# Kernel tuning notes

Measured on AMD Instinct MI355X. Metric: run time of the kernel, lower is better.

The kernel has to match this reference:

```python
import jax, jax.numpy as jnp
import numpy as np

ITER = 18  # prop_time


def _conv3x3(x, w, b):
    # NCHW conv, stride 1, pad 1 (conv_offset_aff)
    y = jax.lax.conv_general_dilated(x, w, window_strides=(1, 1),
                                     padding=((1, 1), (1, 1)),
                                     dimension_numbers=('NCHW', 'OIHW', 'NCHW'))
    return y + b[None, :, None, None]


def _bilinear(img, py, px):
    # img: [H,W]; py/px: [9,H,W] fractional sample coords; zero outside bounds
    H, W = img.shape
    y0 = jnp.floor(py)
    x0 = jnp.floor(px)
    ty = py - y0
    tx = px - x0

    def gather(yf, xf):
        valid = (yf >= 0) & (yf <= H - 1) & (xf >= 0) & (xf <= W - 1)
        yc = jnp.clip(yf, 0, H - 1).astype(jnp.int32)
        xc = jnp.clip(xf, 0, W - 1).astype(jnp.int32)
        return jnp.where(valid, img[yc, xc], 0.0)

    v00 = gather(y0, x0)
    v01 = gather(y0, x0 + 1)
    v10 = gather(y0 + 1, x0)
    v11 = gather(y0 + 1, x0 + 1)
    return (1 - ty) * ((1 - tx) * v00 + tx * v01) + ty * ((1 - tx) * v10 + tx * v11)


def _deform_conv(feat, offset, mask, w9, bias):
    # modulated deformable 3x3 conv, 1 channel, stride 1, pad 1, dil 1
    # offset: [B,18,H,W] in (dy,dx) pairs per kernel tap (torchvision layout)
    B, _, H, W = feat.shape
    off = offset.reshape(B, 9, 2, H, W)
    ky = (jnp.arange(9) // 3 - 1).astype(feat.dtype)  # kernel row offsets
    kx = (jnp.arange(9) % 3 - 1).astype(feat.dtype)   # kernel col offsets
    ys = jnp.arange(H, dtype=feat.dtype)[:, None]
    xs = jnp.arange(W, dtype=feat.dtype)[None, :]
    py = ys[None, None] + ky[None, :, None, None] + off[:, :, 0]  # [B,9,H,W]
    px = xs[None, None] + kx[None, :, None, None] + off[:, :, 1]
    sampled = jax.vmap(_bilinear)(feat[:, 0], py, px)  # [B,9,H,W]
    out = jnp.einsum('bkhw,bkhw,k->bhw', sampled, mask, w9) + bias[0]
    return out[:, None]  # [B,1,H,W]


def _forward(feat_init, guidance, confidence, feat_fix, conv_w, conv_b, w, b):
    conf = jnp.sign(feat_fix) * jax.nn.sigmoid(confidence)
    oa = _conv3x3(guidance, conv_w, conv_b)            # [B,27,H,W]
    offset1 = oa[:, :18].astype(jnp.float16)           # .half() in torch
    aff1 = jax.nn.softmax(oa[:, 18:], axis=1).astype(jnp.float16)
    off_f = offset1.astype(jnp.float32)                # .float() in loop
    aff_f = aff1.astype(jnp.float32)
    w9 = w.reshape(9)

    def step(fr, _):
        fr = (1 - conf) * _deform_conv(fr, off_f, aff_f, w9, b) + conf * feat_fix
        return fr, fr

    pred, list_feat = jax.lax.scan(step, feat_init.astype(jnp.float32), None, length=ITER)
    return pred, list_feat, offset1, aff1


def setup_inputs() -> dict:
    key = jax.random.key(0)
    ks = jax.random.split(key, 6)
    B, H, W = 2, 352, 1216
    feat_init = jax.random.normal(ks[0], (B, 1, H, W), jnp.float32)
    guidance = jax.random.normal(ks[1], (B, 9, H, W), jnp.float32)
    confidence = jax.random.normal(ks[2], (B, 1, H, W), jnp.float32)
    feat_fix = jax.random.normal(ks[3], (B, 1, H, W), jnp.float32)
    # conv_offset_aff params (zero-init in source; small random for a non-trivial baseline)
    conv_w = jax.random.normal(ks[4], (27, 9, 3, 3), jnp.float32) * 0.05
    conv_b = jax.random.normal(ks[5], (27,), jnp.float32) * 0.01
    w = jnp.ones((1, 1, 3, 3), jnp.float32)   # fixed deform-conv weight
    b = jnp.zeros((1,), jnp.float32)          # fixed deform-conv bias
    return {'feat_init': feat_init, 'guidance': guidance, 'confidence': confidence,
            'feat_fix': feat_fix, 'conv_w': conv_w, 'conv_b': conv_b, 'w': w, 'b': b}


def reference(feat_init, guidance, confidence, feat_fix, conv_w, conv_b, w, b):
    return _forward(feat_init, guidance, confidence, feat_fix, conv_w, conv_b, w, b)
```

## Files before the change

kernel.cpp:

```cpp
#include <hip/hip_runtime.h>
#include <hip/hip_fp16.h>

#define HH 352
#define WW 1216
#define HW (HH*WW)
#define NPIX (2*HW)
#define NITER 18
#define PACK_BYTES ((size_t)NPIX * 64)

#define SEGW 256
#define NSEGC ((WW + SEGW - 1) / SEGW)
#define AROW_B 208
#define A_BYTES (256 * AROW_B)
#define B_OFF A_BYTES
#define LDS_BYTES (A_BYTES + 32 * AROW_B)
#define OAROW_B 152

#define SEG 256
#define XHALO 6
#define YHALO 4
#define PROWS 4
#define TROWS (PROWS + 9)
#define TCOLS (SEG + 2*XHALO)
#define NSEG ((WW + SEG - 1) / SEG)

typedef __attribute__((ext_vector_type(8))) short short8;
typedef __attribute__((ext_vector_type(4))) float f32x4;

__device__ __forceinline__ unsigned short f2bf(float f) {
    unsigned u = __float_as_uint(f);
    unsigned r = (u + 0x7fffu + ((u >> 16) & 1u)) >> 16;
    return (unsigned short)r;
}

__global__ __launch_bounds__(256) void conv_mfma_kernel(
    const float* __restrict__ g,
    const float* __restrict__ cw,
    const float* __restrict__ cb,
    const float* __restrict__ confidence,
    const float* __restrict__ feat_fix,
    float* __restrict__ out_off,
    float* __restrict__ out_aff,
    uint4* __restrict__ packed)
{
    __shared__ char lds[LDS_BYTES];

    const int tid = threadIdx.x;
    const int bid = blockIdx.x;
    const int seg = bid % NSEGC;
    const int y   = (bid / NSEGC) % HH;
    const int b   = bid / (NSEGC * HH);
    const int xs  = seg * SEGW;
    const int x   = xs + tid;

    for (int i = tid; i < 32 * 48; i += 256) {
        int n = i / 48;
        int kp = i - n * 48;
        unsigned v = 0;
        if (n < 27) {
            const float* wrow = cw + n * 81;
            int k0 = kp * 2;
            unsigned short h0 = (k0 < 81) ? f2bf(wrow[k0]) : (unsigned short)0;
            unsigned short h1 = (k0 + 1 < 81) ? f2bf(wrow[k0 + 1]) : (unsigned short)0;
            v = (unsigned)h0 | ((unsigned)h1 << 16);
        }
        *(unsigned*)(lds + B_OFF + n * AROW_B + kp * 4) = v;
    }

    {
        const float* gb = g + (size_t)b * 9 * HW;
        unsigned au[48];
#pragma unroll
        for (int j = 0; j < 48; ++j) au[j] = 0;
#pragma unroll
        for (int ci = 0; ci < 9; ++ci)
#pragma unroll
            for (int ty = 0; ty < 3; ++ty) {
                const int row = y + ty - 1;
                const bool vr = ((unsigned)row < HH);
                const float* rp = gb + (size_t)ci * HW + (size_t)(vr ? row : 0) * WW;
                const int cx = xs + tid - 1;
                float L = (vr && (unsigned)cx < WW) ? rp[cx] : 0.f;
                float M = (vr && (unsigned)(cx + 1) < WW) ? rp[cx + 1] : 0.f;
                float R = (vr && (unsigned)(cx + 2) < WW) ? rp[cx + 2] : 0.f;
                const int k = ci * 9 + ty * 3;
                au[(k) >> 1]     |= ((unsigned)f2bf(L)) << (((k) & 1) * 16);
                au[(k + 1) >> 1] |= ((unsigned)f2bf(M)) << (((k + 1) & 1) * 16);
                au[(k + 2) >> 1] |= ((unsigned)f2bf(R)) << (((k + 2) & 1) * 16);
            }
        char* arow = lds + tid * AROW_B;
#pragma unroll
        for (int j = 0; j < 12; ++j)
            *(uint4*)(arow + 16 * j) =
                make_uint4(au[4 * j], au[4 * j + 1], au[4 * j + 2], au[4 * j + 3]);
    }
    __syncthreads();

    const int w = tid >> 6, l = tid & 63;
    const int lrow = l & 15;
    const int lk = (l >> 4) * 8;
    f32x4 acc[4][2];
#pragma unroll
    for (int mt = 0; mt < 4; ++mt)
#pragma unroll
        for (int nt = 0; nt < 2; ++nt)
            acc[mt][nt] = (f32x4){0.f, 0.f, 0.f, 0.f};

#pragma unroll
    for (int kk = 0; kk < 3; ++kk) {
        const int ko = kk * 32 + lk;
        short8 bb0 = *(const short8*)(lds + B_OFF + lrow * AROW_B + ko * 2);
        short8 bb1 = *(const short8*)(lds + B_OFF + (lrow + 16) * AROW_B + ko * 2);
#pragma unroll
        for (int mt = 0; mt < 4; ++mt) {
            short8 aa = *(const short8*)(lds + (w * 64 + mt * 16 + lrow) * AROW_B + ko * 2);
            acc[mt][0] = __builtin_amdgcn_mfma_f32_16x16x32_bf16(aa, bb0, acc[mt][0], 0, 0, 0);
            acc[mt][1] = __builtin_amdgcn_mfma_f32_16x16x32_bf16(aa, bb1, acc[mt][1], 0, 0, 0);
        }
    }
    __syncthreads();

#pragma unroll
    for (int mt = 0; mt < 4; ++mt)
#pragma unroll
        for (int nt = 0; nt < 2; ++nt)
#pragma unroll
            for (int reg = 0; reg < 4; ++reg) {
                int px = w * 64 + mt * 16 + (l >> 4) * 4 + reg;
                int ch = nt * 16 + lrow;
                *(float*)(lds + px * OAROW_B + ch * 4) = acc[mt][nt][reg];
            }
    __syncthreads();

    if (x >= WW) return;
    const int r = y * WW + x;
    const int p = b * HW + r;

    float oa[27];
    {
        const char* orow = lds + tid * OAROW_B;
#pragma unroll
        for (int j = 0; j < 13; ++j) {
            float2 v = *(const float2*)(orow + 8 * j);
            oa[2 * j] = v.x;
            if (2 * j + 1 < 27) oa[2 * j + 1] = v.y;
        }
        oa[26] = *(const float*)(orow + 26 * 4);
#pragma unroll
        for (int c = 0; c < 27; ++c) oa[c] += cb[c];
    }

    __half h[28];
#pragma unroll
    for (int c = 0; c < 18; ++c) h[c] = __float2half(oa[c]);

    float m = oa[18];
#pragma unroll
    for (int c = 19; c < 27; ++c) m = fmaxf(m, oa[c]);
    float e[9], s = 0.f;
#pragma unroll
    for (int k = 0; k < 9; ++k) { e[k] = expf(oa[18 + k] - m); s += e[k]; }
    float inv = 1.f / s;
#pragma unroll
    for (int k = 0; k < 9; ++k) h[18 + k] = __float2half(e[k] * inv);
    h[27] = __float2half(0.f);

#pragma unroll
    for (int c = 0; c < 18; ++c)
        out_off[(size_t)b * 18 * HW + (size_t)c * HW + r] = __half2float(h[c]);
#pragma unroll
    for (int k = 0; k < 9; ++k)
        out_aff[(size_t)b * 9 * HW + (size_t)k * HW + r] = __half2float(h[18 + k]);

    if (packed) {
        float cf = confidence[p];
        float ff = feat_fix[p];
        float sg = (ff > 0.f) ? 1.f : ((ff < 0.f) ? -1.f : 0.f);
        float conf = sg / (1.f + expf(-cf));

        unsigned uu[16];
#pragma unroll
        for (int i = 0; i < 14; ++i)
            uu[i] = (unsigned)__half_as_ushort(h[2 * i]) |
                    ((unsigned)__half_as_ushort(h[2 * i + 1]) << 16);
        uu[14] = __float_as_uint(1.f - conf);
        uu[15] = __float_as_uint(conf * ff);

        uint4* dst = packed + (size_t)p * 4;
        dst[0] = make_uint4(uu[0], uu[1], uu[2], uu[3]);
        dst[1] = make_uint4(uu[4], uu[5], uu[6], uu[7]);
        dst[2] = make_uint4(uu[8], uu[9], uu[10], uu[11]);
        dst[3] = make_uint4(uu[12], uu[13], uu[14], uu[15]);
    }
}

__global__ __launch_bounds__(256) void prop4_kernel(
    const float* __restrict__ src,
    float* __restrict__ dst,
    const uint4* __restrict__ packed,
    const float* __restrict__ w9,
    const float* __restrict__ biasp,
    float* __restrict__ out_pred)
{
    __shared__ float tile[TROWS * TCOLS];

    const int xs = blockIdx.x * SEG;
    const int y0 = blockIdx.y * PROWS;
    const int b  = blockIdx.z;
    const float* sf = src + (size_t)b * HW;

    for (int i = threadIdx.x; i < TROWS * TCOLS; i += 256) {
        int rr = i / TCOLS;
        int cc = i - rr * TCOLS;
        int gy = y0 - YHALO + rr;
        int gx = xs - XHALO + cc;
        float v = 0.f;
        if ((unsigned)gy < HH && (unsigned)gx < WW)
            v = sf[(size_t)gy * WW + gx];
        tile[i] = v;
    }
    __syncthreads();

    const int x = xs + threadIdx.x;
    if (x >= WW) return;
    const float bias = biasp[0];

#pragma unroll 1
    for (int ty = 0; ty < PROWS; ++ty) {
        const int y = y0 + ty;
        const int r = y * WW + x;
        const int p = b * HW + r;

        const uint4* pk = packed + (size_t)p * 4;
        uint4 q0 = pk[0], q1 = pk[1], q2 = pk[2], q3 = pk[3];
        unsigned uu[14] = {q0.x, q0.y, q0.z, q0.w, q1.x, q1.y, q1.z, q1.w,
                           q2.x, q2.y, q2.z, q2.w, q3.x, q3.y};
        float hv[27];
#pragma unroll
        for (int i = 0; i < 13; ++i) {
            hv[2 * i]     = __half2float(__ushort_as_half((unsigned short)(uu[i] & 0xffff)));
            hv[2 * i + 1] = __half2float(__ushort_as_half((unsigned short)(uu[i] >> 16)));
        }
        hv[26] = __half2float(__ushort_as_half((unsigned short)(uu[13] & 0xffff)));
        float cm1 = __uint_as_float(q3.z);
        float cff = __uint_as_float(q3.w);

        float acc = 0.f;
#pragma unroll
        for (int k = 0; k < 9; ++k) {
            float py = (float)y + (float)(k / 3 - 1) + hv[2 * k];
            float px = (float)x + (float)(k % 3 - 1) + hv[2 * k + 1];
            float y0f = floorf(py), x0f = floorf(px);
            float tyf = py - y0f, txf = px - x0f;
            int iy = (int)y0f, ix = (int)x0f;

            int ly = iy - y0 + YHALO;
            int lx = ix - xs + XHALO;
            float v00, v01, v10, v11;
            if ((unsigned)ly < (TROWS - 1) && (unsigned)lx < (TCOLS - 1)) {
                const float* t0 = &tile[ly * TCOLS + lx];
                v00 = t0[0];     v01 = t0[1];
                v10 = t0[TCOLS]; v11 = t0[TCOLS + 1];
            } else {
                bool vy0 = ((unsigned)iy < HH), vy1 = ((unsigned)(iy + 1) < HH);
                bool vx0 = ((unsigned)ix < WW), vx1 = ((unsigned)(ix + 1) < WW);
                v00 = (vy0 && vx0) ? sf[(size_t)iy * WW + ix] : 0.f;
                v01 = (vy0 && vx1) ? sf[(size_t)iy * WW + ix + 1] : 0.f;
                v10 = (vy1 && vx0) ? sf[(size_t)(iy + 1) * WW + ix] : 0.f;
                v11 = (vy1 && vx1) ? sf[(size_t)(iy + 1) * WW + ix + 1] : 0.f;
            }
            float top = (1.f - txf) * v00 + txf * v01;
            float bot = (1.f - txf) * v10 + txf * v11;
            float sv = (1.f - tyf) * top + tyf * bot;
            acc = fmaf(sv * hv[18 + k], w9[k], acc);
        }
        float dc = acc + bias;
        float fr = fmaf(cm1, dc, cff);

        dst[p] = fr;
        if (out_pred) out_pred[p] = fr;
    }
}

__global__ __launch_bounds__(256) void prop_kernel(
    const float* __restrict__ src,
    float* __restrict__ dst,
    const float* __restrict__ off,
    const float* __restrict__ aff,
    const float* __restrict__ confidence,
    const float* __restrict__ feat_fix,
    const float* __restrict__ w9,
    const float* __restrict__ biasp,
    float* __restrict__ out_pred)
{
    int p = blockIdx.x * 256 + threadIdx.x;
    if (p >= NPIX) return;
    int b = p / HW;
    int r = p - b * HW;
    int y = r / WW;
    int x = r - y * WW;

    const float* offb = off + (size_t)b * 18 * HW + r;
    const float* affb = aff + (size_t)b * 9 * HW + r;
    const float* sf = src + (size_t)b * HW;

    float acc = 0.f;
#pragma unroll
    for (int k = 0; k < 9; ++k) {
        float dy = offb[(size_t)(2 * k) * HW];
        float dx = offb[(size_t)(2 * k + 1) * HW];
        float af = affb[(size_t)k * HW];
        float py = (float)y + (float)(k / 3 - 1) + dy;
        float px = (float)x + (float)(k % 3 - 1) + dx;
        float y0f = floorf(py), x0f = floorf(px);
        float ty = py - y0f, tx = px - x0f;
        int iy = (int)y0f, ix = (int)x0f;
        bool vy0 = ((unsigned)iy < HH), vy1 = ((unsigned)(iy + 1) < HH);
        bool vx0 = ((unsigned)ix < WW), vx1 = ((unsigned)(ix + 1) < WW);
        float v00 = (vy0 && vx0) ? sf[(size_t)iy * WW + ix] : 0.f;
        float v01 = (vy0 && vx1) ? sf[(size_t)iy * WW + ix + 1] : 0.f;
        float v10 = (vy1 && vx0) ? sf[(size_t)(iy + 1) * WW + ix] : 0.f;
        float v11 = (vy1 && vx1) ? sf[(size_t)(iy + 1) * WW + ix + 1] : 0.f;
        float top = (1.f - tx) * v00 + tx * v01;
        float bot = (1.f - tx) * v10 + tx * v11;
        float sv = (1.f - ty) * top + ty * bot;
        acc = fmaf(sv * af, w9[k], acc);
    }
    float dc = acc + biasp[0];

    float cf = confidence[p];
    float ffv = feat_fix[p];
    float sg = (ffv > 0.f) ? 1.f : ((ffv < 0.f) ? -1.f : 0.f);
    float conf = sg / (1.f + expf(-cf));
    float fr = (1.f - conf) * dc + conf * ffv;

    dst[p] = fr;
    if (out_pred) out_pred[p] = fr;
}

extern "C" void kernel_launch(void* const* d_in, const int* in_sizes, int n_in,
                              void* d_out, int out_size, void* d_ws, size_t ws_size,
                              hipStream_t stream) {
    const float* feat_init  = (const float*)d_in[0];
    const float* guidance   = (const float*)d_in[1];
    const float* confidence = (const float*)d_in[2];
    const float* feat_fix   = (const float*)d_in[3];
    const float* conv_w     = (const float*)d_in[4];
    const float* conv_b     = (const float*)d_in[5];
    const float* w          = (const float*)d_in[6];
    const float* bias       = (const float*)d_in[7];

    float* outf = (float*)d_out;
    float* out_pred = outf;
    float* out_list = outf + (size_t)NPIX;
    float* out_off  = outf + (size_t)19 * NPIX;
    float* out_aff  = outf + (size_t)37 * NPIX;

    bool use_pack = (ws_size >= PACK_BYTES);
    uint4* packed = use_pack ? (uint4*)d_ws : nullptr;

    conv_mfma_kernel<<<NSEGC * HH * 2, 256, 0, stream>>>(
        guidance, conv_w, conv_b, confidence, feat_fix,
        out_off, out_aff, packed);

    dim3 pgrid(NSEG, HH / PROWS, 2);
    int blocks = (NPIX + 255) / 256;
    const float* src = feat_init;
    for (int it = 0; it < NITER; ++it) {
        float* dstf = out_list + (size_t)it * NPIX;
        float* predp = (it == NITER - 1) ? out_pred : nullptr;
        if (use_pack) {
            prop4_kernel<<<pgrid, 256, 0, stream>>>(
                src, dstf, packed, w, bias, predp);
        } else {
            prop_kernel<<<blocks, 256, 0, stream>>>(
                src, dstf, out_off, out_aff, confidence, feat_fix, w, bias, predp);
        }
        src = dstf;
    }
}
```

Before: 372.8 us.

## Fold weights and bias into packed data, double prop rows, use packed bf16 converts

The conv kernel now uses the hardware v_cvt_pk_bf16_f32 instruction and a fast interior path without bounds checks. It also pre-multiplies the affinity by the deform weights and folds the bias into the packed constant, which removes per-iteration weight loads and multiplies from the propagation kernel. The propagation kernel processes 8 rows per block instead of 4, which reduces halo overhead. It also loads tiles row-wise, reads LDS pairs as float2 and uses an FMA-form lerp. Rounding changes slightly because the weight product is stored in fp16 and the bilinear blend uses FMAs.

```diff
diff --git a/kernel.cpp b/kernel.cpp
--- a/kernel.cpp
+++ b/kernel.cpp
@@ -19,7 +19,7 @@
 #define SEG 256
 #define XHALO 6
 #define YHALO 4
-#define PROWS 4
+#define PROWS 8
 #define TROWS (PROWS + 9)
 #define TCOLS (SEG + 2*XHALO)
 #define NSEG ((WW + SEG - 1) / SEG)
@@ -27,10 +27,16 @@
 typedef __attribute__((ext_vector_type(8))) short short8;
 typedef __attribute__((ext_vector_type(4))) float f32x4;
 
-__device__ __forceinline__ unsigned short f2bf(float f) {
-    unsigned u = __float_as_uint(f);
-    unsigned r = (u + 0x7fffu + ((u >> 16) & 1u)) >> 16;
-    return (unsigned short)r;
+__device__ __forceinline__ unsigned cvt_pk_bf16(float lo, float hi) {
+    unsigned r;
+    asm("v_cvt_pk_bf16_f32 %0, %1, %2" : "=v"(r) : "v"(lo), "v"(hi));
+    return r;
+}
+
+__device__ __forceinline__ float2 lds2(const float* p) {
+    float2 v;
+    __builtin_memcpy(&v, p, 8);
+    return v;
 }
 
 __global__ __launch_bounds__(256) void conv_mfma_kernel(
@@ -39,6 +45,8 @@
     const float* __restrict__ cb,
     const float* __restrict__ confidence,
     const float* __restrict__ feat_fix,
+    const float* __restrict__ w9,
+    const float* __restrict__ biasp,
     float* __restrict__ out_off,
     float* __restrict__ out_aff,
     uint4* __restrict__ packed)
@@ -60,9 +68,9 @@
         if (n < 27) {
             const float* wrow = cw + n * 81;
             int k0 = kp * 2;
-            unsigned short h0 = (k0 < 81) ? f2bf(wrow[k0]) : (unsigned short)0;
-            unsigned short h1 = (k0 + 1 < 81) ? f2bf(wrow[k0 + 1]) : (unsigned short)0;
-            v = (unsigned)h0 | ((unsigned)h1 << 16);
+            float f0 = (k0 < 81) ? wrow[k0] : 0.f;
+            float f1 = (k0 + 1 < 81) ? wrow[k0 + 1] : 0.f;
+            v = cvt_pk_bf16(f0, f1);
         }
         *(unsigned*)(lds + B_OFF + n * AROW_B + kp * 4) = v;
     }
@@ -72,22 +80,53 @@
         unsigned au[48];
 #pragma unroll
         for (int j = 0; j < 48; ++j) au[j] = 0;
-#pragma unroll
-        for (int ci = 0; ci < 9; ++ci)
-#pragma unroll
-            for (int ty = 0; ty < 3; ++ty) {
-                const int row = y + ty - 1;
-                const bool vr = ((unsigned)row < HH);
-                const float* rp = gb + (size_t)ci * HW + (size_t)(vr ? row : 0) * WW;
-                const int cx = xs + tid - 1;
-                float L = (vr && (unsigned)cx < WW) ? rp[cx] : 0.f;
-                float M = (vr && (unsigned)(cx + 1) < WW) ? rp[cx + 1] : 0.f;
-                float R = (vr && (unsigned)(cx + 2) < WW) ? rp[cx + 2] : 0.f;
-                const int k = ci * 9 + ty * 3;
-                au[(k) >> 1]     |= ((unsigned)f2bf(L)) << (((k) & 1) * 16);
-                au[(k + 1) >> 1] |= ((unsigned)f2bf(M)) << (((k + 1) & 1) * 16);
-                au[(k + 2) >> 1] |= ((unsigned)f2bf(R)) << (((k + 2) & 1) * 16);
+        float held = 0.f;
+
+        bool interior = (y >= 1) & (y <= HH - 2) & (x >= 1) & (x <= WW - 2);
+        if (interior) {
+            const float* c0 = gb + (size_t)(y - 1) * WW + (x - 1);
+#pragma unroll
+            for (int ci = 0; ci < 9; ++ci) {
+                const float* cp = c0 + (size_t)ci * HW;
+#pragma unroll
+                for (int ty = 0; ty < 3; ++ty) {
+                    float L = cp[ty * WW], M = cp[ty * WW + 1], R = cp[ty * WW + 2];
+                    const int k = ci * 9 + ty * 3;
+                    if ((k & 1) == 0) {
+                        au[k >> 1] = cvt_pk_bf16(L, M);
+                        held = R;
+                    } else {
+                        au[(k - 1) >> 1] = cvt_pk_bf16(held, L);
+                        au[(k + 1) >> 1] = cvt_pk_bf16(M, R);
+                    }
+                }
             }
+        } else {
+#pragma unroll
+            for (int ci = 0; ci < 9; ++ci) {
+                const float* cp = gb + (size_t)ci * HW;
+#pragma unroll
+                for (int ty = 0; ty < 3; ++ty) {
+                    const int row = y + ty - 1;
+                    const bool vr = ((unsigned)row < HH);
+                    const float* rp = cp + (size_t)(vr ? row : 0) * WW;
+                    const int cx = x - 1;
+                    float L = (vr && (unsigned)cx < WW) ? rp[cx] : 0.f;
+                    float M = (vr && (unsigned)(cx + 1) < WW) ? rp[cx + 1] : 0.f;
+                    float R = (vr && (unsigned)(cx + 2) < WW) ? rp[cx + 2] : 0.f;
+                    const int k = ci * 9 + ty * 3;
+                    if ((k & 1) == 0) {
+                        au[k >> 1] = cvt_pk_bf16(L, M);
+                        held = R;
+                    } else {
+                        au[(k - 1) >> 1] = cvt_pk_bf16(held, L);
+                        au[(k + 1) >> 1] = cvt_pk_bf16(M, R);
+                    }
+                }
+            }
+        }
+        au[40] = cvt_pk_bf16(held, 0.f);
+
         char* arow = lds + tid * AROW_B;
 #pragma unroll
         for (int j = 0; j < 12; ++j)
@@ -150,7 +189,7 @@
         for (int c = 0; c < 27; ++c) oa[c] += cb[c];
     }
 
-    __half h[28];
+    __half h[27];
 #pragma unroll
     for (int c = 0; c < 18; ++c) h[c] = __float2half(oa[c]);
 
@@ -163,7 +202,6 @@
     float inv = 1.f / s;
 #pragma unroll
     for (int k = 0; k < 9; ++k) h[18 + k] = __float2half(e[k] * inv);
-    h[27] = __float2half(0.f);
 
 #pragma unroll
     for (int c = 0; c < 18; ++c)
@@ -177,14 +215,26 @@
         float ff = feat_fix[p];
         float sg = (ff > 0.f) ? 1.f : ((ff < 0.f) ? -1.f : 0.f);
         float conf = sg / (1.f + expf(-cf));
+        float cm1 = 1.f - conf;
+        float bias = biasp[0];
+
+        __half hw[9];
+#pragma unroll
+        for (int k = 0; k < 9; ++k)
+            hw[k] = __float2half(__half2float(h[18 + k]) * w9[k]);
 
         unsigned uu[16];
 #pragma unroll
-        for (int i = 0; i < 14; ++i)
+        for (int i = 0; i < 9; ++i)
             uu[i] = (unsigned)__half_as_ushort(h[2 * i]) |
                     ((unsigned)__half_as_ushort(h[2 * i + 1]) << 16);
-        uu[14] = __float_as_uint(1.f - conf);
-        uu[15] = __float_as_uint(conf * ff);
+#pragma unroll
+        for (int j = 0; j < 4; ++j)
+            uu[9 + j] = (unsigned)__half_as_ushort(hw[2 * j]) |
+                        ((unsigned)__half_as_ushort(hw[2 * j + 1]) << 16);
+        uu[13] = (unsigned)__half_as_ushort(hw[8]);
+        uu[14] = __float_as_uint(cm1);
+        uu[15] = __float_as_uint(fmaf(cm1, bias, conf * ff));
 
         uint4* dst = packed + (size_t)p * 4;
         dst[0] = make_uint4(uu[0], uu[1], uu[2], uu[3]);
@@ -194,12 +244,10 @@
     }
 }
 
-__global__ __launch_bounds__(256) void prop4_kernel(
+__global__ __launch_bounds__(256) void prop8_kernel(
     const float* __restrict__ src,
     float* __restrict__ dst,
     const uint4* __restrict__ packed,
-    const float* __restrict__ w9,
-    const float* __restrict__ biasp,
     float* __restrict__ out_pred)
 {
     __shared__ float tile[TROWS * TCOLS];
@@ -209,27 +257,25 @@
     const int b  = blockIdx.z;
     const float* sf = src + (size_t)b * HW;
 
-    for (int i = threadIdx.x; i < TROWS * TCOLS; i += 256) {
-        int rr = i / TCOLS;
-        int cc = i - rr * TCOLS;
-        int gy = y0 - YHALO + rr;
-        int gx = xs - XHALO + cc;
-        float v = 0.f;
-        if ((unsigned)gy < HH && (unsigned)gx < WW)
-            v = sf[(size_t)gy * WW + gx];
-        tile[i] = v;
+#pragma unroll 1
+    for (int rr = 0; rr < TROWS; ++rr) {
+        const int gy = y0 - YHALO + rr;
+        const bool vr = ((unsigned)gy < HH);
+        const float* rp = sf + (size_t)(vr ? gy : 0) * WW;
+        for (int cc = threadIdx.x; cc < TCOLS; cc += 256) {
+            const int gx = xs - XHALO + cc;
+            tile[rr * TCOLS + cc] = (vr && (unsigned)gx < WW) ? rp[gx] : 0.f;
+        }
     }
     __syncthreads();
 
     const int x = xs + threadIdx.x;
     if (x >= WW) return;
-    const float bias = biasp[0];
 
 #pragma unroll 1
     for (int ty = 0; ty < PROWS; ++ty) {
         const int y = y0 + ty;
-        const int r = y * WW + x;
-        const int p = b * HW + r;
+        const int p = b * HW + y * WW + x;
 
         const uint4* pk = packed + (size_t)p * 4;
         uint4 q0 = pk[0], q1 = pk[1], q2 = pk[2], q3 = pk[3];
@@ -242,16 +288,16 @@
             hv[2 * i + 1] = __half2float(__ushort_as_half((unsigned short)(uu[i] >> 16)));
         }
         hv[26] = __half2float(__ushort_as_half((unsigned short)(uu[13] & 0xffff)));
-        float cm1 = __uint_as_float(q3.z);
-        float cff = __uint_as_float(q3.w);
+        const float cm1 = __uint_as_float(q3.z);
+        const float cff = __uint_as_float(q3.w);
 
         float acc = 0.f;
 #pragma unroll
         for (int k = 0; k < 9; ++k) {
-            float py = (float)y + (float)(k / 3 - 1) + hv[2 * k];
-            float px = (float)x + (float)(k % 3 - 1) + hv[2 * k + 1];
-            float y0f = floorf(py), x0f = floorf(px);
-            float tyf = py - y0f, txf = px - x0f;
+            float py  = (float)(y + k / 3 - 1) + hv[2 * k];
+            float pxx = (float)(x + k % 3 - 1) + hv[2 * k + 1];
+            float y0f = floorf(py), x0f = floorf(pxx);
+            float tyf = py - y0f, txf = pxx - x0f;
             int iy = (int)y0f, ix = (int)x0f;
 
             int ly = iy - y0 + YHALO;
@@ -259,8 +305,9 @@
             float v00, v01, v10, v11;
             if ((unsigned)ly < (TROWS - 1) && (unsigned)lx < (TCOLS - 1)) {
                 const float* t0 = &tile[ly * TCOLS + lx];
-                v00 = t0[0];     v01 = t0[1];
-                v10 = t0[TCOLS]; v11 = t0[TCOLS + 1];
+                float2 tp = lds2(t0);
+                float2 bo = lds2(t0 + TCOLS);
+                v00 = tp.x; v01 = tp.y; v10 = bo.x; v11 = bo.y;
             } else {
                 bool vy0 = ((unsigned)iy < HH), vy1 = ((unsigned)(iy + 1) < HH);
                 bool vx0 = ((unsigned)ix < WW), vx1 = ((unsigned)(ix + 1) < WW);
@@ -269,13 +316,12 @@
                 v10 = (vy1 && vx0) ? sf[(size_t)(iy + 1) * WW + ix] : 0.f;
                 v11 = (vy1 && vx1) ? sf[(size_t)(iy + 1) * WW + ix + 1] : 0.f;
             }
-            float top = (1.f - txf) * v00 + txf * v01;
-            float bot = (1.f - txf) * v10 + txf * v11;
-            float sv = (1.f - tyf) * top + tyf * bot;
-            acc = fmaf(sv * hv[18 + k], w9[k], acc);
-        }
-        float dc = acc + bias;
-        float fr = fmaf(cm1, dc, cff);
+            float top = fmaf(txf, v01 - v00, v00);
+            float bot = fmaf(txf, v11 - v10, v10);
+            float sv  = fmaf(tyf, bot - top, top);
+            acc = fmaf(sv, hv[18 + k], acc);
+        }
+        float fr = fmaf(cm1, acc, cff);
 
         dst[p] = fr;
         if (out_pred) out_pred[p] = fr;
@@ -360,7 +406,7 @@
     uint4* packed = use_pack ? (uint4*)d_ws : nullptr;
 
     conv_mfma_kernel<<<NSEGC * HH * 2, 256, 0, stream>>>(
-        guidance, conv_w, conv_b, confidence, feat_fix,
+        guidance, conv_w, conv_b, confidence, feat_fix, w, bias,
         out_off, out_aff, packed);
 
     dim3 pgrid(NSEG, HH / PROWS, 2);
@@ -370,8 +416,7 @@
         float* dstf = out_list + (size_t)it * NPIX;
         float* predp = (it == NITER - 1) ? out_pred : nullptr;
         if (use_pack) {
-            prop4_kernel<<<pgrid, 256, 0, stream>>>(
-                src, dstf, packed, w, bias, predp);
+            prop8_kernel<<<pgrid, 256, 0, stream>>>(src, dstf, packed, predp);
         } else {
             prop_kernel<<<blocks, 256, 0, stream>>>(
                 src, dstf, out_off, out_aff, confidence, feat_fix, w, bias, predp);
```

After: 516.6 us. 38.6% more time.
